# Kernel optimization log

Measured on AMD Instinct MI355X. Metric: run time of the kernel, lower is better.

The kernel has to match this reference:

```python
import jax, jax.numpy as jnp
import numpy as np


def _mk_mat(rows):
    # rows: list of 3 lists of (B,) arrays, written as matrix rows.
    # torch code stacks rows at dim=2, which transposes: replicate that.
    M = jnp.stack([jnp.stack(r, axis=1) for r in rows], axis=1)  # (B,3,3) written-rows
    return jnp.swapaxes(M, 1, 2)  # matches torch.stack(..., dim=2)


def _compose_mats(affine, scale, translate, shear):
    B = affine.shape[0]
    one = jnp.ones((B,), affine.dtype)
    zero = jnp.zeros((B,), affine.dtype)
    cx, sx = jnp.cos(affine[:, 0]), jnp.sin(affine[:, 0])
    cy, sy = jnp.cos(affine[:, 1]), jnp.sin(affine[:, 1])
    cz, sz = jnp.cos(affine[:, 2]), jnp.sin(affine[:, 2])
    rot_x = _mk_mat([[one, zero, zero], [zero, cx, -sx], [zero, sx, cx]])
    rot_y = _mk_mat([[cy, zero, sy], [zero, one, zero], [-sy, zero, cy]])
    rot_z = _mk_mat([[cz, -sz, zero], [sz, cz, zero], [zero, zero, one]])
    scale_m = _mk_mat([[scale[:, 0], zero, zero], [zero, scale[:, 1], zero], [zero, zero, scale[:, 2]]])
    t = jnp.tan(shear)
    shear_m = _mk_mat([[one, t[:, 0], t[:, 1]], [t[:, 2], one, t[:, 3]], [t[:, 4], t[:, 5], one]])
    trans = translate[:, :, None]  # (B,3,1)
    mat3 = shear_m @ (scale_m @ (rot_z @ (rot_y @ rot_x)))  # (B,3,3)
    inv3 = jnp.linalg.inv(mat3)
    mat = jnp.concatenate([mat3, trans], axis=-1)  # (B,3,4)
    inv_trans = jnp.matmul(-inv3, trans)
    inv_mat = jnp.concatenate([inv3, inv_trans], axis=-1)
    return mat, inv_mat


def _affine_grid(mat, D, H, W):
    # torch affine_grid, align_corners=False: coord_i = (2*i+1)/n - 1
    dt = mat.dtype
    xs = (jnp.arange(W, dtype=dt) + 0.5) * (2.0 / W) - 1.0
    ys = (jnp.arange(H, dtype=dt) + 0.5) * (2.0 / H) - 1.0
    zs = (jnp.arange(D, dtype=dt) + 0.5) * (2.0 / D) - 1.0
    zz, yy, xx = jnp.meshgrid(zs, ys, xs, indexing='ij')
    coords = jnp.stack([xx, yy, zz], axis=-1)  # (D,H,W,3) in (x,y,z) order
    grid = jnp.einsum('bkj,dhwj->bdhwk', mat[:, :, :3], coords) + mat[:, None, None, None, :, 3]
    return grid  # (B,D,H,W,3)


def _grid_sample_trilinear(src, grid):
    # torch grid_sample, mode='bilinear' (trilinear in 3D), padding zeros, align_corners=False
    B, C, D, H, W = src.shape
    ix = (grid[..., 0] + 1.0) * (W * 0.5) - 0.5
    iy = (grid[..., 1] + 1.0) * (H * 0.5) - 0.5
    iz = (grid[..., 2] + 1.0) * (D * 0.5) - 0.5
    fx, fy, fz = jnp.floor(ix), jnp.floor(iy), jnp.floor(iz)
    wx, wy, wz = ix - fx, iy - fy, iz - fz  # fractional weights
    x0, y0, z0 = fx.astype(jnp.int32), fy.astype(jnp.int32), fz.astype(jnp.int32)
    x1, y1, z1 = x0 + 1, y0 + 1, z0 + 1
    N = D * H * W
    src_flat = src.reshape(B, C, N)

    def gather(z, y, x):
        valid = (x >= 0) & (x < W) & (y >= 0) & (y < H) & (z >= 0) & (z < D)
        xi = jnp.clip(x, 0, W - 1)
        yi = jnp.clip(y, 0, H - 1)
        zi = jnp.clip(z, 0, D - 1)
        idx = ((zi * H + yi) * W + xi).reshape(B, 1, N)
        v = jnp.take_along_axis(src_flat, jnp.broadcast_to(idx, (B, C, N)), axis=2)
        return v * valid.reshape(B, 1, N).astype(src.dtype)

    def w(a):
        return a.reshape(B, 1, N)

    out = (gather(z0, y0, x0) * w((1 - wz) * (1 - wy) * (1 - wx))
           + gather(z0, y0, x1) * w((1 - wz) * (1 - wy) * wx)
           + gather(z0, y1, x0) * w((1 - wz) * wy * (1 - wx))
           + gather(z0, y1, x1) * w((1 - wz) * wy * wx)
           + gather(z1, y0, x0) * w(wz * (1 - wy) * (1 - wx))
           + gather(z1, y0, x1) * w(wz * (1 - wy) * wx)
           + gather(z1, y1, x0) * w(wz * wy * (1 - wx))
           + gather(z1, y1, x1) * w(wz * wy * wx))
    return out.reshape(B, C, D, H, W)


def setup_inputs() -> dict:
    key = jax.random.key(0)
    k1, k2, k3, k4, k5 = jax.random.split(key, 5)
    B, C, D, H, W = 2, 1, 192, 192, 192
    src = jax.random.normal(k1, (B, C, D, H, W), dtype=jnp.float32)
    affine = jax.random.uniform(k2, (B, 3), dtype=jnp.float32)
    scale = jax.random.uniform(k3, (B, 3), dtype=jnp.float32)
    translate = jax.random.uniform(k4, (B, 3), dtype=jnp.float32)
    shear = jax.random.uniform(k5, (B, 6), dtype=jnp.float32)
    return {"src": src, "affine": affine, "scale": scale, "translate": translate, "shear": shear}


def reference(src, affine, scale, translate, shear):
    B, C, D, H, W = src.shape
    mat, inv_mat = _compose_mats(affine, scale, translate, shear)
    grid = _affine_grid(mat, D, H, W)
    warped = _grid_sample_trilinear(src, grid)
    return warped, mat, inv_mat
```

## Files before the change

### kernel.cpp

```cpp
#include <hip/hip_runtime.h>
#include <math.h>

#define Bv 2
#define Dv 192
#define Hv 192
#define Wv 192
#define Nv (Dv*Hv*Wv)
#define NOUT (Bv*Nv)


__device__ __forceinline__ void mm3(const float a[3][3], const float b[3][3], float c[3][3]) {
#pragma unroll
    for (int i = 0; i < 3; ++i)
#pragma unroll
        for (int j = 0; j < 3; ++j)
            c[i][j] = a[i][0]*b[0][j] + a[i][1]*b[1][j] + a[i][2]*b[2][j];
}

__global__ void compose_mats_kernel(const float* __restrict__ affine,
                                    const float* __restrict__ scale,
                                    const float* __restrict__ translate,
                                    const float* __restrict__ shear,
                                    float* __restrict__ mats_out) {
    int b = threadIdx.x;
    if (b >= Bv) return;

    float ax = affine[b*3+0], ay = affine[b*3+1], az = affine[b*3+2];
    float cx = cosf(ax), sx = sinf(ax);
    float cy = cosf(ay), sy = sinf(ay);
    float cz = cosf(az), sz = sinf(az);

    float rx[3][3] = {{1.f,0.f,0.f},{0.f,cx,sx},{0.f,-sx,cx}};
    float ry[3][3] = {{cy,0.f,-sy},{0.f,1.f,0.f},{sy,0.f,cy}};
    float rz[3][3] = {{cz,sz,0.f},{-sz,cz,0.f},{0.f,0.f,1.f}};

    float t0 = tanf(shear[b*6+0]), t1 = tanf(shear[b*6+1]), t2 = tanf(shear[b*6+2]);
    float t3 = tanf(shear[b*6+3]), t4 = tanf(shear[b*6+4]), t5 = tanf(shear[b*6+5]);
    float sh[3][3] = {{1.f,t2,t4},{t0,1.f,t5},{t1,t3,1.f}};

    float s0 = scale[b*3+0], s1 = scale[b*3+1], s2 = scale[b*3+2];

    float m1[3][3], m2[3][3], m3s[3][3], mat3[3][3];
    mm3(ry, rx, m1);
    mm3(rz, m1, m2);
#pragma unroll
    for (int j = 0; j < 3; ++j) { m3s[0][j] = s0*m2[0][j]; m3s[1][j] = s1*m2[1][j]; m3s[2][j] = s2*m2[2][j]; }
    mm3(sh, m3s, mat3);

    float tr0 = translate[b*3+0], tr1 = translate[b*3+1], tr2 = translate[b*3+2];

    float a00 = mat3[0][0], a01 = mat3[0][1], a02 = mat3[0][2];
    float a10 = mat3[1][0], a11 = mat3[1][1], a12 = mat3[1][2];
    float a20 = mat3[2][0], a21 = mat3[2][1], a22 = mat3[2][2];
    float c00 =  (a11*a22 - a12*a21);
    float c01 = -(a10*a22 - a12*a20);
    float c02 =  (a10*a21 - a11*a20);
    float det = a00*c00 + a01*c01 + a02*c02;
    float rdet = 1.0f / det;
    float inv3[3][3];
    inv3[0][0] = c00*rdet;
    inv3[0][1] = (a02*a21 - a01*a22)*rdet;
    inv3[0][2] = (a01*a12 - a02*a11)*rdet;
    inv3[1][0] = c01*rdet;
    inv3[1][1] = (a00*a22 - a02*a20)*rdet;
    inv3[1][2] = (a02*a10 - a00*a12)*rdet;
    inv3[2][0] = c02*rdet;
    inv3[2][1] = (a01*a20 - a00*a21)*rdet;
    inv3[2][2] = (a00*a11 - a01*a10)*rdet;

    float* mo = mats_out + b*12;
#pragma unroll
    for (int i = 0; i < 3; ++i) {
        mo[i*4+0] = mat3[i][0]; mo[i*4+1] = mat3[i][1]; mo[i*4+2] = mat3[i][2];
    }
    mo[0*4+3] = tr0; mo[1*4+3] = tr1; mo[2*4+3] = tr2;

    float* io = mats_out + 24 + b*12;
#pragma unroll
    for (int i = 0; i < 3; ++i) {
        io[i*4+0] = inv3[i][0]; io[i*4+1] = inv3[i][1]; io[i*4+2] = inv3[i][2];
        io[i*4+3] = -(inv3[i][0]*tr0 + inv3[i][1]*tr1 + inv3[i][2]*tr2);
    }
}

__device__ __forceinline__ float2 ld2(const float* p) {
    float2 r;
    __builtin_memcpy(&r, p, 8);
    return r;
}

__global__ __launch_bounds__(512) void warp_kernel(const float* __restrict__ src,
                                                   const float* __restrict__ mats,
                                                   float* __restrict__ out) {
    __shared__ float tileO[512];

    int t    = threadIdx.x;
    int lane = t & 63;
    int wv   = t >> 6;
    int wvx  = wv & 3;
    int wvy  = wv >> 2;

    int lx = (lane & 3)        + (wvx << 2);
    int ly = ((lane >> 2) & 3) + (wvy << 2);
    int lz = lane >> 4;

    int W0 = blockIdx.x * 16;
    int H0 = blockIdx.y * 8;
    int zt = blockIdx.z;
    int b  = zt / (Dv/4);
    int Z0 = (zt % (Dv/4)) * 4;

    int w = W0 + lx, h = H0 + ly, z = Z0 + lz;

    const float* M = mats + b*12;
    float m00 = M[0], m01 = M[1],  m02 = M[2],  m03 = M[3];
    float m10 = M[4], m11 = M[5],  m12 = M[6],  m13 = M[7];
    float m20 = M[8], m21 = M[9],  m22 = M[10], m23 = M[11];

    float Cx = 96.0f*(m03 - m00 - m01 - m02) + 95.5f;
    float Cy = 96.0f*(m13 - m10 - m11 - m12) + 95.5f;
    float Cz = 96.0f*(m23 - m20 - m21 - m22) + 95.5f;

    float fw = w + 0.5f, fh = h + 0.5f, fzc = z + 0.5f;
    float ix = fmaf(m00, fw, fmaf(m01, fh, fmaf(m02, fzc, Cx)));
    float iy = fmaf(m10, fw, fmaf(m11, fh, fmaf(m12, fzc, Cy)));
    float iz = fmaf(m20, fw, fmaf(m21, fh, fmaf(m22, fzc, Cz)));

    float flx = floorf(ix), fly = floorf(iy), flz = floorf(iz);
    float wx = ix - flx, wy = iy - fly, wz = iz - flz;
    int x0 = (int)flx, y0 = (int)fly, z0 = (int)flz;

    const float* sb = src + (size_t)b * Nv;

    float acc = 0.0f;

    bool all_in = ((unsigned)x0 < (unsigned)(Wv-1)) &
                  ((unsigned)y0 < (unsigned)(Hv-1)) &
                  ((unsigned)z0 < (unsigned)(Dv-1));

    if (all_in) {
        const float* p = sb + ((z0*Hv + y0)*Wv + x0);
        const float* q = p + Hv*Wv;
        float2 v00 = ld2(p);
        float2 v01 = ld2(p + Wv);
        float2 v10 = ld2(q);
        float2 v11 = ld2(q + Wv);
        float c00 = fmaf(wx, v00.y - v00.x, v00.x);
        float c01 = fmaf(wx, v01.y - v01.x, v01.x);
        float c10 = fmaf(wx, v10.y - v10.x, v10.x);
        float c11 = fmaf(wx, v11.y - v11.x, v11.x);
        float c0  = fmaf(wy, c01 - c00, c00);
        float c1  = fmaf(wy, c11 - c10, c10);
        acc = fmaf(wz, c1 - c0, c0);
    } else {
        int x1 = x0 + 1, y1 = y0 + 1, z1 = z0 + 1;
        bool all_out = (x1 < 0) | (x0 >= Wv) | (y1 < 0) | (y0 >= Hv) | (z1 < 0) | (z0 >= Dv);
        if (!all_out) {
            auto gather = [&](int zz, int yy, int xx) -> float {
                bool valid = ((unsigned)xx < (unsigned)Wv) &
                             ((unsigned)yy < (unsigned)Hv) &
                             ((unsigned)zz < (unsigned)Dv);
                int xi = min(max(xx, 0), Wv-1);
                int yi = min(max(yy, 0), Hv-1);
                int zi = min(max(zz, 0), Dv-1);
                float val = sb[(zi*Hv + yi)*Wv + xi];
                return valid ? val : 0.0f;
            };
            float owx = 1.0f - wx, owy = 1.0f - wy, owz = 1.0f - wz;
            acc  = gather(z0, y0, x0) * (owz*owy*owx);
            acc += gather(z0, y0, x1) * (owz*owy*wx);
            acc += gather(z0, y1, x0) * (owz*wy*owx);
            acc += gather(z0, y1, x1) * (owz*wy*wx);
            acc += gather(z1, y0, x0) * (wz*owy*owx);
            acc += gather(z1, y0, x1) * (wz*owy*wx);
            acc += gather(z1, y1, x0) * (wz*wy*owx);
            acc += gather(z1, y1, x1) * (wz*wy*wx);
        }
    }

    int s = lx + (ly << 4) + (lz << 7);
    tileO[s ^ (lz << 2)] = acc;
    __syncthreads();

    float v = tileO[t ^ (((t >> 7) & 3) << 2)];

    int w2 = W0 + (t & 15);
    int h2 = H0 + ((t >> 4) & 7);
    int z2 = Z0 + (t >> 7);
    __builtin_nontemporal_store(v, &out[((size_t)(b*Dv + z2)*Hv + h2)*Wv + w2]);
}

extern "C" void kernel_launch(void* const* d_in, const int* in_sizes, int n_in,
                              void* d_out, int out_size, void* d_ws, size_t ws_size,
                              hipStream_t stream) {
    const float* src       = (const float*)d_in[0];
    const float* affine    = (const float*)d_in[1];
    const float* scale     = (const float*)d_in[2];
    const float* translate = (const float*)d_in[3];
    const float* shear     = (const float*)d_in[4];

    float* out  = (float*)d_out;
    float* mats = out + NOUT;

    compose_mats_kernel<<<1, 64, 0, stream>>>(affine, scale, translate, shear, mats);

    dim3 grid(Wv/16, Hv/8, (Dv/4)*Bv);
    warp_kernel<<<grid, 512, 0, stream>>>(src, mats, out);
}
```

Before: 60.50 us.

## Stage each block's source footprint in LDS before trilinear sampling

Each block computes the bounding box of the source region its output tile maps to, cooperatively loads that box into a 32KB shared-memory stage with float4 row loads, and then does the eight-corner trilinear fetches from LDS. The goal is to swap scattered global gathers for coalesced row loads and more data reuse. When the footprint exceeds the stage capacity, the old direct-gather path is used. The cost is extra shared memory (lower occupancy), an added barrier, and possibly loading more voxels than needed when the transform stretches the footprint.

Measured after the change: 114.0 us. 1.88x slower.

```diff
diff --git a/kernel.cpp b/kernel.cpp
--- a/kernel.cpp
+++ b/kernel.cpp
@@ -7,6 +7,8 @@
 #define Wv 192
 #define Nv (Dv*Hv*Wv)
 #define NOUT (Bv*Nv)
+
+#define STAGE_CAP 8192
 
 
 __device__ __forceinline__ void mm3(const float a[3][3], const float b[3][3], float c[3][3]) {
@@ -88,10 +90,16 @@
     __builtin_memcpy(&r, p, 8);
     return r;
 }
+__device__ __forceinline__ float4 ld4(const float* p) {
+    float4 r;
+    __builtin_memcpy(&r, p, 16);
+    return r;
+}
 
 __global__ __launch_bounds__(512) void warp_kernel(const float* __restrict__ src,
                                                    const float* __restrict__ mats,
                                                    float* __restrict__ out) {
+    __shared__ float stage[STAGE_CAP];
     __shared__ float tileO[512];
 
     int t    = threadIdx.x;
@@ -132,49 +140,119 @@
 
     const float* sb = src + (size_t)b * Nv;
 
+    float cxv = fmaf(m00, W0+8.0f, fmaf(m01, H0+4.0f, fmaf(m02, Z0+2.0f, Cx)));
+    float cyv = fmaf(m10, W0+8.0f, fmaf(m11, H0+4.0f, fmaf(m12, Z0+2.0f, Cy)));
+    float czv = fmaf(m20, W0+8.0f, fmaf(m21, H0+4.0f, fmaf(m22, Z0+2.0f, Cz)));
+    float hxv = 7.5f*fabsf(m00) + 3.5f*fabsf(m01) + 1.5f*fabsf(m02);
+    float hyv = 7.5f*fabsf(m10) + 3.5f*fabsf(m11) + 1.5f*fabsf(m12);
+    float hzv = 7.5f*fabsf(m20) + 3.5f*fabsf(m21) + 1.5f*fabsf(m22);
+
+    int bx0 = (int)floorf(cxv - hxv) - 1;
+    int by0 = (int)floorf(cyv - hyv) - 1;
+    int bz0 = (int)floorf(czv - hzv) - 1;
+    int ex  = (int)floorf(cxv + hxv) + 3 - bx0;
+    int ey  = (int)floorf(cyv + hyv) + 3 - by0;
+    int ez  = (int)floorf(czv + hzv) + 3 - bz0;
+
+    int ldw   = ex | 1;
+    int nrows = ey * ez;
+    int vol   = nrows * ldw;
+
     float acc = 0.0f;
 
-    bool all_in = ((unsigned)x0 < (unsigned)(Wv-1)) &
-                  ((unsigned)y0 < (unsigned)(Hv-1)) &
-                  ((unsigned)z0 < (unsigned)(Dv-1));
-
-    if (all_in) {
-        const float* p = sb + ((z0*Hv + y0)*Wv + x0);
-        const float* q = p + Hv*Wv;
-        float2 v00 = ld2(p);
-        float2 v01 = ld2(p + Wv);
-        float2 v10 = ld2(q);
-        float2 v11 = ld2(q + Wv);
-        float c00 = fmaf(wx, v00.y - v00.x, v00.x);
-        float c01 = fmaf(wx, v01.y - v01.x, v01.x);
-        float c10 = fmaf(wx, v10.y - v10.x, v10.x);
-        float c11 = fmaf(wx, v11.y - v11.x, v11.x);
+    if (vol <= STAGE_CAP) {
+        int tidr = t >> 2;
+        int cb0  = (t & 3) << 2;
+        for (int r = tidr; r < nrows; r += 128) {
+            int dz = r / ey;
+            int dy = r - dz*ey;
+            int gy = by0 + dy, gz = bz0 + dz;
+            bool rowok = ((unsigned)gy < (unsigned)Hv) & ((unsigned)gz < (unsigned)Dv);
+            int gyc = min(max(gy, 0), Hv-1);
+            int gzc = min(max(gz, 0), Dv-1);
+            const float* rowp = sb + (gzc*Hv + gyc)*Wv;
+            int rowbase = r * ldw;
+            for (int cb = cb0; cb < ex; cb += 16) {
+                int gx = bx0 + cb;
+                if (rowok & (gx >= 0) & (gx + 3 < Wv)) {
+                    float4 v = ld4(rowp + gx);
+                    stage[rowbase + cb + 0] = v.x;
+                    stage[rowbase + cb + 1] = v.y;
+                    stage[rowbase + cb + 2] = v.z;
+                    stage[rowbase + cb + 3] = v.w;
+                } else {
+#pragma unroll
+                    for (int k = 0; k < 4; ++k) {
+                        int gxk = gx + k;
+                        bool vk = rowok & ((unsigned)gxk < (unsigned)Wv);
+                        int gxc = min(max(gxk, 0), Wv-1);
+                        float val = rowp[gxc];
+                        if (cb + k < ex) stage[rowbase + cb + k] = vk ? val : 0.0f;
+                    }
+                }
+            }
+        }
+        __syncthreads();
+
+        int lix = min(max(x0 - bx0, 0), ex - 2);
+        int liy = min(max(y0 - by0, 0), ey - 2);
+        int liz = min(max(z0 - bz0, 0), ez - 2);
+        int pl   = ey * ldw;
+        int base = (liz * ey + liy) * ldw + lix;
+        float v000 = stage[base],            v001 = stage[base + 1];
+        float v010 = stage[base + ldw],      v011 = stage[base + ldw + 1];
+        float v100 = stage[base + pl],       v101 = stage[base + pl + 1];
+        float v110 = stage[base + pl + ldw], v111 = stage[base + pl + ldw + 1];
+
+        float c00 = fmaf(wx, v001 - v000, v000);
+        float c01 = fmaf(wx, v011 - v010, v010);
+        float c10 = fmaf(wx, v101 - v100, v100);
+        float c11 = fmaf(wx, v111 - v110, v110);
         float c0  = fmaf(wy, c01 - c00, c00);
         float c1  = fmaf(wy, c11 - c10, c10);
         acc = fmaf(wz, c1 - c0, c0);
     } else {
-        int x1 = x0 + 1, y1 = y0 + 1, z1 = z0 + 1;
-        bool all_out = (x1 < 0) | (x0 >= Wv) | (y1 < 0) | (y0 >= Hv) | (z1 < 0) | (z0 >= Dv);
-        if (!all_out) {
-            auto gather = [&](int zz, int yy, int xx) -> float {
-                bool valid = ((unsigned)xx < (unsigned)Wv) &
-                             ((unsigned)yy < (unsigned)Hv) &
-                             ((unsigned)zz < (unsigned)Dv);
-                int xi = min(max(xx, 0), Wv-1);
-                int yi = min(max(yy, 0), Hv-1);
-                int zi = min(max(zz, 0), Dv-1);
-                float val = sb[(zi*Hv + yi)*Wv + xi];
-                return valid ? val : 0.0f;
-            };
-            float owx = 1.0f - wx, owy = 1.0f - wy, owz = 1.0f - wz;
-            acc  = gather(z0, y0, x0) * (owz*owy*owx);
-            acc += gather(z0, y0, x1) * (owz*owy*wx);
-            acc += gather(z0, y1, x0) * (owz*wy*owx);
-            acc += gather(z0, y1, x1) * (owz*wy*wx);
-            acc += gather(z1, y0, x0) * (wz*owy*owx);
-            acc += gather(z1, y0, x1) * (wz*owy*wx);
-            acc += gather(z1, y1, x0) * (wz*wy*owx);
-            acc += gather(z1, y1, x1) * (wz*wy*wx);
+        bool all_in = ((unsigned)x0 < (unsigned)(Wv-1)) &
+                      ((unsigned)y0 < (unsigned)(Hv-1)) &
+                      ((unsigned)z0 < (unsigned)(Dv-1));
+        if (all_in) {
+            const float* p = sb + ((z0*Hv + y0)*Wv + x0);
+            const float* q = p + Hv*Wv;
+            float2 v00 = ld2(p);
+            float2 v01 = ld2(p + Wv);
+            float2 v10 = ld2(q);
+            float2 v11 = ld2(q + Wv);
+            float c00 = fmaf(wx, v00.y - v00.x, v00.x);
+            float c01 = fmaf(wx, v01.y - v01.x, v01.x);
+            float c10 = fmaf(wx, v10.y - v10.x, v10.x);
+            float c11 = fmaf(wx, v11.y - v11.x, v11.x);
+            float c0  = fmaf(wy, c01 - c00, c00);
+            float c1  = fmaf(wy, c11 - c10, c10);
+            acc = fmaf(wz, c1 - c0, c0);
+        } else {
+            int x1 = x0 + 1, y1 = y0 + 1, z1 = z0 + 1;
+            bool all_out = (x1 < 0) | (x0 >= Wv) | (y1 < 0) | (y0 >= Hv) | (z1 < 0) | (z0 >= Dv);
+            if (!all_out) {
+                auto gather = [&](int zz, int yy, int xx) -> float {
+                    bool valid = ((unsigned)xx < (unsigned)Wv) &
+                                 ((unsigned)yy < (unsigned)Hv) &
+                                 ((unsigned)zz < (unsigned)Dv);
+                    int xi = min(max(xx, 0), Wv-1);
+                    int yi = min(max(yy, 0), Hv-1);
+                    int zi = min(max(zz, 0), Dv-1);
+                    float val = sb[(zi*Hv + yi)*Wv + xi];
+                    return valid ? val : 0.0f;
+                };
+                float owx = 1.0f - wx, owy = 1.0f - wy, owz = 1.0f - wz;
+                acc  = gather(z0, y0, x0) * (owz*owy*owx);
+                acc += gather(z0, y0, x0+1) * (owz*owy*wx);
+                acc += gather(z0, y0+1, x0) * (owz*wy*owx);
+                acc += gather(z0, y0+1, x0+1) * (owz*wy*wx);
+                acc += gather(z0+1, y0, x0) * (wz*owy*owx);
+                acc += gather(z0+1, y0, x0+1) * (wz*owy*wx);
+                acc += gather(z0+1, y0+1, x0) * (wz*wy*owx);
+                acc += gather(z0+1, y0+1, x0+1) * (wz*wy*wx);
+            }
         }
     }
 
```
